# Kernel optimization log

Hardware: AMD Instinct MI355X
Metric: run time of the kernel (lower is better)

Reference implementation:

```python
import jax, jax.numpy as jnp
import numpy as np


def setup_inputs() -> dict:
    key = jax.random.key(0)
    x = jax.random.normal(key, (32, 64, 64, 64), dtype=jnp.float32)
    return {"x": x, "num_zeros": 2}


def reference(x, num_zeros):
    # ZeroWeave: interleave `num_zeros` zeros between every pair of pixels
    # along both spatial dims (equivalent to the gather_nd over
    # concat([x, zeros_like(x)]) with the precomputed index tensor).
    # x: [B, C, H, W] -> [B, C, H*s - num_zeros, W*s - num_zeros], s = num_zeros + 1
    s = num_zeros + 1
    B, C, H, W = x.shape
    out_h = H * s - num_zeros
    out_w = W * s - num_zeros
    out = jnp.zeros((B, C, out_h, out_w), dtype=x.dtype)
    out = out.at[:, :, ::s, ::s].set(x)
    return out
```

## Files before the change

kernel.cpp:

```cpp
#include <hip/hip_runtime.h>


constexpr int S   = 3;
constexpr int H   = 64;
constexpr int W   = 64;
constexpr int OH  = H * S - (S - 1);
constexpr int OW  = W * S - (S - 1);
constexpr int PLANE_IN  = H * W;
constexpr int N_OUT = 32 * 64 * OH * OW;
constexpr int N4    = N_OUT / 4;

__global__ __launch_bounds__(256) void ZeroWeave_89601607729830_kernel(
    const float* __restrict__ x, float* __restrict__ out) {
    int i = blockIdx.x * blockDim.x + threadIdx.x;
    if (i >= N4) return;

    int base = i * 4;
    float4 v;
    float* vp = reinterpret_cast<float*>(&v);

#pragma unroll
    for (int j = 0; j < 4; ++j) {
        int f  = base + j;
        int w  = f % OW;
        int t  = f / OW;
        int h  = t % OH;
        int bc = t / OH;
        float val = 0.0f;
        if ((h % S) == 0 && (w % S) == 0) {
            val = x[bc * PLANE_IN + (h / S) * W + (w / S)];
        }
        vp[j] = val;
    }

    reinterpret_cast<float4*>(out)[i] = v;
}

extern "C" void kernel_launch(void* const* d_in, const int* in_sizes, int n_in,
                              void* d_out, int out_size, void* d_ws, size_t ws_size,
                              hipStream_t stream) {
    const float* x = (const float*)d_in[0];
    float* out = (float*)d_out;

    constexpr int BLOCK = 256;
    int grid = (N4 + BLOCK - 1) / BLOCK;
    ZeroWeave_89601607729830_kernel<<<grid, BLOCK, 0, stream>>>(x, out);
}
```

Baseline: 345.6 us.

## Stage each input plane in LDS, one block per plane, magic-number div/mod

Each block now handles one (b,c) plane. It loads the 64x64 input into shared memory with float4 loads, then writes the 190x190 output plane as float4 stores. The per-element 64-bit-free div/mod by 190 and 3 are replaced by multiply-shift magic constants, which removes integer division cost and scattered global gathers. The trade-offs are a __syncthreads per block and fewer blocks (2048), each with a longer serial loop.

```diff
diff --git a/kernel.cpp b/kernel.cpp
--- a/kernel.cpp
+++ b/kernel.cpp
@@ -1,39 +1,58 @@
 #include <hip/hip_runtime.h>
 
 
-constexpr int S   = 3;
-constexpr int H   = 64;
-constexpr int W   = 64;
-constexpr int OH  = H * S - (S - 1);
-constexpr int OW  = W * S - (S - 1);
-constexpr int PLANE_IN  = H * W;
-constexpr int N_OUT = 32 * 64 * OH * OW;
-constexpr int N4    = N_OUT / 4;
+constexpr int H = 64, W = 64;
+constexpr int OH = 190, OW = 190;
+constexpr int PLANE_IN = H * W;
+constexpr int PLANE_OUT4 = OH * OW / 4;
+constexpr int NPLANES = 32 * 64;
+constexpr int BLOCK = 256;
+constexpr int FULL_ITERS = PLANE_OUT4 / BLOCK;
+constexpr int TAIL = PLANE_OUT4 - FULL_ITERS * BLOCK;
 
-__global__ __launch_bounds__(256) void ZeroWeave_89601607729830_kernel(
+__global__ __launch_bounds__(BLOCK) void ZeroWeave_89601607729830_kernel(
     const float* __restrict__ x, float* __restrict__ out) {
-    int i = blockIdx.x * blockDim.x + threadIdx.x;
-    if (i >= N4) return;
+    __shared__ float lds[PLANE_IN];
 
-    int base = i * 4;
-    float4 v;
-    float* vp = reinterpret_cast<float*>(&v);
+    const int bc  = blockIdx.x;
+    const int tid = threadIdx.x;
 
+    {
+        const float4* xp = reinterpret_cast<const float4*>(x + bc * PLANE_IN);
+        float4* l4 = reinterpret_cast<float4*>(lds);
 #pragma unroll
-    for (int j = 0; j < 4; ++j) {
-        int f  = base + j;
-        int w  = f % OW;
-        int t  = f / OW;
-        int h  = t % OH;
-        int bc = t / OH;
-        float val = 0.0f;
-        if ((h % S) == 0 && (w % S) == 0) {
-            val = x[bc * PLANE_IN + (h / S) * W + (w / S)];
+        for (int k = 0; k < PLANE_IN / 4 / BLOCK; ++k)
+            l4[k * BLOCK + tid] = xp[k * BLOCK + tid];
+    }
+    __syncthreads();
+
+    float4* op = reinterpret_cast<float4*>(out) + bc * PLANE_OUT4;
+
+    auto emit = [&](int q) {
+        const int e0 = q * 4;
+        float4 v;
+        float* vp = reinterpret_cast<float*>(&v);
+#pragma unroll
+        for (int j = 0; j < 4; ++j) {
+            unsigned e = (unsigned)(e0 + j);
+            unsigned h = (e * 44151u) >> 23;
+            unsigned w = e - h * 190u;
+            unsigned h3 = (h * 171u) >> 9;
+            unsigned hm = h - h3 * 3u;
+            unsigned w3 = (w * 171u) >> 9;
+            unsigned wm = w - w3 * 3u;
+            float val = 0.0f;
+            if ((hm | wm) == 0u) val = lds[(h3 << 6) + w3];
+            vp[j] = val;
         }
-        vp[j] = val;
-    }
+        op[q] = v;
+    };
 
-    reinterpret_cast<float4*>(out)[i] = v;
+#pragma unroll 4
+    for (int k = 0; k < FULL_ITERS; ++k)
+        emit(k * BLOCK + tid);
+    if (tid < TAIL)
+        emit(FULL_ITERS * BLOCK + tid);
 }
 
 extern "C" void kernel_launch(void* const* d_in, const int* in_sizes, int n_in,
@@ -42,7 +61,5 @@
     const float* x = (const float*)d_in[0];
     float* out = (float*)d_out;
 
-    constexpr int BLOCK = 256;
-    int grid = (N4 + BLOCK - 1) / BLOCK;
-    ZeroWeave_89601607729830_kernel<<<grid, BLOCK, 0, stream>>>(x, out);
+    ZeroWeave_89601607729830_kernel<<<NPLANES, BLOCK, 0, stream>>>(x, out);
 }
```

After: 328.4 us. 5.0% less time.
